# Performance work log

Measured on AMD Instinct MI355X. Metric: run time of the kernel, lower is better.

Reference implementation:

```python
import jax, jax.numpy as jnp
import numpy as np

D_MODEL = 512
H = 8
D_K = D_MODEL // H


def setup_inputs() -> dict:
    key = jax.random.key(0)
    ks = jax.random.split(key, 11)
    B, S = 2, 2048
    scale = 1.0 / np.sqrt(D_MODEL)
    return {
        "q": jax.random.normal(ks[0], (B, S, D_MODEL), jnp.float32),
        "v": jax.random.normal(ks[1], (B, S, D_MODEL), jnp.float32),
        "k": jax.random.normal(ks[2], (B, S, D_MODEL), jnp.float32),
        "w_q": jax.random.normal(ks[3], (D_MODEL, D_MODEL), jnp.float32) * scale,
        "b_q": jnp.zeros((D_MODEL,), jnp.float32),
        "w_k": jax.random.normal(ks[4], (D_MODEL, D_MODEL), jnp.float32) * scale,
        "b_k": jnp.zeros((D_MODEL,), jnp.float32),
        "w_v": jax.random.normal(ks[5], (D_MODEL, D_MODEL), jnp.float32) * scale,
        "b_v": jnp.zeros((D_MODEL,), jnp.float32),
        "w_o": jax.random.normal(ks[6], (D_MODEL, D_MODEL), jnp.float32) * scale,
        "b_o": jnp.zeros((D_MODEL,), jnp.float32),
    }


def reference(q, v, k, w_q, b_q, w_k, b_k, w_v, b_v, w_o, b_o):
    B, S, _ = q.shape
    # projections (nn.Linear: x @ W.T + b)
    query = q @ w_q.T + b_q
    key_t = k @ w_k.T + b_k
    value = v @ w_v.T + b_v
    # split heads: [B, S, H, D_K] -> [B, H, S, D_K]
    query = query.reshape(B, S, H, D_K).transpose(0, 2, 1, 3)
    key_t = key_t.reshape(B, S, H, D_K).transpose(0, 2, 1, 3)
    value = value.reshape(B, S, H, D_K).transpose(0, 2, 1, 3)
    # unfused attention: full [B, H, S, S] score matrix
    scores = jnp.einsum("bhqd,bhkd->bhqk", query, key_t) / jnp.sqrt(
        jnp.asarray(D_K, query.dtype)
    )
    attn = jax.nn.softmax(scores, axis=-1)  # dropout inactive in eval
    x = jnp.einsum("bhqk,bhkd->bhqd", attn, value)
    # merge heads and output projection
    x = x.transpose(0, 2, 1, 3).reshape(B, S, D_MODEL)
    return x @ w_o.T + b_o
```

## Files before the change

### kernel.cpp

```cpp
#include <hip/hip_runtime.h>
#include <hip/hip_bf16.h>


typedef __attribute__((ext_vector_type(8))) short short8;
typedef __attribute__((ext_vector_type(4))) short short4v;
typedef __attribute__((ext_vector_type(4))) float f32x4;
typedef __attribute__((ext_vector_type(2))) unsigned int uint2v;

#define DM 512
#define SEQ 2048
#define NROW 4096
#define LOG2E 1.44269504088896341f
#define MFMA(a, b, c) __builtin_amdgcn_mfma_f32_16x16x32_bf16(a, b, c, 0, 0, 0)
#define FENCE() __asm__ __volatile__("" ::: "memory")
#define WAITVM(n) __builtin_amdgcn_s_waitcnt(0x3F70 | (n))
#define WAITLGKM0() __builtin_amdgcn_s_waitcnt(0xC07F)
#define BARRIER() do { FENCE(); __builtin_amdgcn_s_barrier(); FENCE(); } while (0)

#if __has_builtin(__builtin_amdgcn_exp2f)
#define EXP2(x) __builtin_amdgcn_exp2f(x)
#else
#define EXP2(x) exp2f(x)
#endif

__device__ __forceinline__ float bf_bits2f(short s) {
    unsigned int u = ((unsigned int)(unsigned short)s) << 16;
    return __builtin_bit_cast(float, u);
}
__device__ __forceinline__ short f2bf_r(float f) {
    unsigned int u = __builtin_bit_cast(unsigned int, f) + 0x8000u;
    return (short)(u >> 16);
}
__device__ __forceinline__ unsigned int pack_bf16(float lo, float hi) {
    unsigned int ul = __builtin_bit_cast(unsigned int, lo) + 0x8000u;
    unsigned int uh = __builtin_bit_cast(unsigned int, hi) + 0x8000u;
    return __builtin_amdgcn_perm(uh, ul, 0x07060302u);
}

__device__ __forceinline__ void gload_lds16(const void* src, void* lds_dst) {
    __builtin_amdgcn_global_load_lds(
        (const __attribute__((address_space(1))) unsigned int*)src,
        (__attribute__((address_space(3))) unsigned int*)lds_dst, 16, 0, 0);
}

template <int ROWS, int NW, int SH>
__device__ __forceinline__ void stage_tile(const short* __restrict__ gsrc, size_t gstride,
                                           short* lds, int wave, int lane) {
    constexpr int ISSUES = ROWS * 8 / (64 * NW);
    #pragma unroll
    for (int i = 0; i < ISSUES; i++) {
        const int blk = i * NW + wave;
        const int g = blk * 64 + lane;
        const int row = g >> 3;
        const int cb = (g & 7) ^ ((row >> SH) & 7);
        gload_lds16(gsrc + (size_t)row * gstride + cb * 8, lds + (size_t)blk * 512);
    }
}

__device__ __forceinline__ bool detect_f32(const unsigned int* __restrict__ q, int* cnt_lds) {
    if (threadIdx.x == 0) *cnt_lds = 0;
    __syncthreads();
    int local = 0;
    for (int i = threadIdx.x; i < 1024; i += blockDim.x) {
        unsigned int lo = q[i] & 0x7FFFu;
        if (lo >= 0x3000u && lo < 0x4400u) local++;
    }
    if (local) atomicAdd(cnt_lds, local);
    __syncthreads();
    return *cnt_lds < 512;
}

struct ConvArgs { const void* src[11]; short* dst[11]; int n[11]; };
__global__ void convert_all(ConvArgs a) {
    __shared__ int cnt;
    const bool f32m = detect_f32((const unsigned int*)a.src[0], &cnt);
    if (!f32m) return;
    const int tid = blockIdx.x * 256 + threadIdx.x;
    const int stride = gridDim.x * 256;
    for (int s = 0; s < 11; s++) {
        const float4* sp = (const float4*)a.src[s];
        short4v* dp = (short4v*)a.dst[s];
        const int n4 = a.n[s] >> 2;
        for (int i = tid; i < n4; i += stride) {
            float4 v = sp[i];
            short4v o;
            o[0] = f2bf_r(v.x); o[1] = f2bf_r(v.y);
            o[2] = f2bf_r(v.z); o[3] = f2bf_r(v.w);
            dp[i] = o;
        }
    }
}

template <int MT>
__device__ __forceinline__ void gemm_core(const short* __restrict__ A,
                                          const short* __restrict__ W,
                                          int m0, int n0, short* Alds, short* Blds,
                                          int wave, int lane, f32x4 (&acc)[MT / 64][4]) {
    const int rc = lane & 15, quad = lane >> 4;
    const short* Ag = A + (size_t)m0 * DM;
    const short* Bg = W + (size_t)n0 * DM;
    constexpr int ABUF = MT * 64, BBUF = 64 * 64;
    constexpr int IN = MT * 8 / 256 + 2;
    constexpr int NITER = DM / 64;

    stage_tile<MT, 4, 0>(Ag, DM, Alds, wave, lane);
    stage_tile<64, 4, 0>(Bg, DM, Blds, wave, lane);
    stage_tile<MT, 4, 0>(Ag + 64, DM, Alds + ABUF, wave, lane);
    stage_tile<64, 4, 0>(Bg + 64, DM, Blds + BBUF, wave, lane);

    #pragma unroll
    for (int i = 0; i < NITER; i++) {
        const int cur = i % 3;
        if (i + 1 < NITER) WAITVM(IN); else WAITVM(0);
        BARRIER();
        if (i + 2 < NITER) {
            const int nb = (i + 2) % 3;
            stage_tile<MT, 4, 0>(Ag + (i + 2) * 64, DM, Alds + nb * ABUF, wave, lane);
            stage_tile<64, 4, 0>(Bg + (i + 2) * 64, DM, Blds + nb * BBUF, wave, lane);
        }
        const short* Ac = Alds + cur * ABUF;
        const short* Bc = Blds + cur * BBUF;
        #pragma unroll
        for (int h = 0; h < 2; h++) {
            short8 bf[4];
            #pragma unroll
            for (int nt = 0; nt < 4; nt++) {
                const int br = nt * 16 + rc;
                bf[nt] = *(const short8*)&Bc[br * 64 + (((quad + 4 * h) ^ (br & 7)) * 8)];
            }
            #pragma unroll
            for (int ms = 0; ms < MT / 64; ms++) {
                const int ar = wave * (MT / 4) + ms * 16 + rc;
                short8 af = *(const short8*)&Ac[ar * 64 + (((quad + 4 * h) ^ (ar & 7)) * 8)];
                #pragma unroll
                for (int nt = 0; nt < 4; nt++)
                    acc[ms][nt] = MFMA(af, bf[nt], acc[ms][nt]);
            }
        }
    }
}

struct QKVArgs {
    const short* Araw[3]; const short* Wraw[3]; const short* Braw[3];
    const short* Acv[3];  const short* Wcv[3];  const short* Bcv[3];
    short* Cq; short* Ck; short* Cv;
    const unsigned int* qraw;
};
__global__ __launch_bounds__(256, 2) void qkv_gemm(QKVArgs args) {
    __shared__ __align__(16) short Alds[3][128 * 64];
    __shared__ __align__(16) short Blds[3][64 * 64];
    __shared__ int cnt;
    const bool f32m = detect_f32(args.qraw, &cnt);
    const int z = blockIdx.z;
    const short* A    = f32m ? args.Acv[z] : args.Araw[z];
    const short* W    = f32m ? args.Wcv[z] : args.Wraw[z];
    const short* bias = f32m ? args.Bcv[z] : args.Braw[z];
    const int wave = threadIdx.x >> 6, lane = threadIdx.x & 63;
    const int rc = lane & 15, quad = lane >> 4;
    const int m0 = blockIdx.x * 128, n0 = blockIdx.y * 64;

    f32x4 acc[2][4] = {};
    gemm_core<128>(A, W, m0, n0, &Alds[0][0], &Blds[0][0], wave, lane, acc);

    if (z == 2) {
        const int hh = n0 >> 6;
        #pragma unroll
        for (int ms = 0; ms < 2; ms++) {
            const int mw = m0 + wave * 32 + ms * 16;
            const int b = mw >> 11, sb = (mw & 2047) + quad * 4;
            #pragma unroll
            for (int nt = 0; nt < 4; nt++) {
                const int d = nt * 16 + rc;
                const float bv = bf_bits2f(bias[n0 + d]);
                short4v pk;
                #pragma unroll
                for (int r = 0; r < 4; r++) pk[r] = f2bf_r(acc[ms][nt][r] + bv);
                *(short4v*)(args.Cv + ((size_t)((b * 8 + hh) * 64 + d)) * SEQ + sb) = pk;
            }
        }
    } else {
        short* C = (z == 0) ? args.Cq : args.Ck;
        const float sc = (z == 0) ? (0.125f * LOG2E) : 1.0f;
        #pragma unroll
        for (int ms = 0; ms < 2; ms++) {
            const int mw = m0 + wave * 32 + ms * 16;
            #pragma unroll
            for (int nt = 0; nt < 4; nt++) {
                const int col = n0 + nt * 16 + rc;
                const float bv = bf_bits2f(bias[col]);
                #pragma unroll
                for (int r = 0; r < 4; r++)
                    C[(size_t)(mw + quad * 4 + r) * DM + col] = f2bf_r((acc[ms][nt][r] + bv) * sc);
            }
        }
    }
}

__global__ __launch_bounds__(256, 2) void out_gemm(
    const short* __restrict__ A, const short* __restrict__ Wraw,
    const short* __restrict__ Wcv, const short* __restrict__ Braw,
    const short* __restrict__ Bcv, void* __restrict__ Cout,
    const unsigned int* __restrict__ qraw) {
    __shared__ __align__(16) short Alds[3][64 * 64];
    __shared__ __align__(16) short Blds[3][64 * 64];
    __shared__ int cnt;
    const bool f32m = detect_f32(qraw, &cnt);
    const short* W    = f32m ? Wcv : Wraw;
    const short* bias = f32m ? Bcv : Braw;
    const int wave = threadIdx.x >> 6, lane = threadIdx.x & 63;
    const int rc = lane & 15, quad = lane >> 4;
    const int m0 = blockIdx.x * 64, n0 = blockIdx.y * 64;
    f32x4 acc[1][4] = {};
    gemm_core<64>(A, W, m0, n0, &Alds[0][0], &Blds[0][0], wave, lane, acc);
    const int mw = m0 + wave * 16;
    #pragma unroll
    for (int nt = 0; nt < 4; nt++) {
        const int col = n0 + nt * 16 + rc;
        const float bv = bf_bits2f(bias[col]);
        #pragma unroll
        for (int r = 0; r < 4; r++) {
            const size_t idx = (size_t)(mw + quad * 4 + r) * DM + col;
            const float val = acc[0][nt][r] + bv;
            if (f32m) ((float*)Cout)[idx] = val;
            else      ((short*)Cout)[idx] = f2bf_r(val);
        }
    }
}

__global__ __launch_bounds__(256, 2) void attn_kernel(
    const short* __restrict__ Q, const short* __restrict__ K,
    const short* __restrict__ Vt, float* __restrict__ Opart,
    float* __restrict__ Lpart)
{
    __shared__ __align__(16) short Klds[3][64 * 64];
    __shared__ __align__(16) short Vlds[3][64 * 64];
    __shared__ __align__(16) short Plds[4][32 * 72];

    const int wave = threadIdx.x >> 6, lane = threadIdx.x & 63;
    const int rc = lane & 15, quad = lane >> 4;
    const int bh = blockIdx.y, z = blockIdx.z;
    const size_t baseQ = (size_t)(bh >> 3) * SEQ * DM + (size_t)(bh & 7) * 64;
    const short* Qb = Q + baseQ;
    const short* Kb = K + baseQ + (size_t)(z * 1024) * DM;
    const short* Vb = Vt + (size_t)bh * 64 * SEQ + z * 1024;
    const int q0 = blockIdx.x * 128 + wave * 32;

    short8 qa[2][2];
    #pragma unroll
    for (int ms = 0; ms < 2; ms++)
        #pragma unroll
        for (int h = 0; h < 2; h++)
            qa[ms][h] = *(const short8*)(Qb + (size_t)(q0 + ms * 16 + rc) * DM + h * 32 + quad * 8);

    short8 ones;
    #pragma unroll
    for (int j = 0; j < 8; j++) ones[j] = (short)0x3F80;

    f32x4 o[2][4] = {};
    f32x4 lsum[2] = {};
    short* Pw = &Plds[wave][0];

    int koff[4][2], voff[4][2];
    #pragma unroll
    for (int kt = 0; kt < 4; kt++) {
        const int row = rc * 4 + kt;
        #pragma unroll
        for (int h = 0; h < 2; h++)
            koff[kt][h] = row * 64 + (((quad + 4 * h) ^ (rc & 7)) * 8);
    }
    #pragma unroll
    for (int dt = 0; dt < 4; dt++) {
        const int row = dt * 16 + rc;
        #pragma unroll
        for (int h = 0; h < 2; h++)
            voff[dt][h] = row * 64 + (((quad + 4 * h) ^ (row & 7)) * 8);
    }

    stage_tile<64, 4, 2>(Kb, DM, &Klds[0][0], wave, lane);
    stage_tile<64, 4, 0>(Vb, SEQ, &Vlds[0][0], wave, lane);
    stage_tile<64, 4, 2>(Kb + (size_t)64 * DM, DM, &Klds[1][0], wave, lane);
    stage_tile<64, 4, 0>(Vb + 64, SEQ, &Vlds[1][0], wave, lane);

    #pragma unroll
    for (int it = 0; it < 16; it++) {
        const int cur = it % 3;
        if (it + 1 < 16) WAITVM(4); else WAITVM(0);
        BARRIER();
        if (it + 2 < 16) {
            const int k0n = (it + 2) * 64;
            const int nb = (it + 2) % 3;
            stage_tile<64, 4, 2>(Kb + (size_t)k0n * DM, DM, &Klds[nb][0], wave, lane);
            stage_tile<64, 4, 0>(Vb + k0n, SEQ, &Vlds[nb][0], wave, lane);
        }
        const short* Kt = &Klds[cur][0];
        const short* Vl = &Vlds[cur][0];

        short8 kf[4][2];
        #pragma unroll
        for (int kt = 0; kt < 4; kt++)
            #pragma unroll
            for (int h = 0; h < 2; h++)
                kf[kt][h] = *(const short8*)&Kt[koff[kt][h]];
        f32x4 s[2][4];
        #pragma unroll
        for (int ms = 0; ms < 2; ms++)
            #pragma unroll
            for (int kt = 0; kt < 4; kt++) {
                f32x4 t = {};
                t = MFMA(qa[ms][0], kf[kt][0], t);
                t = MFMA(qa[ms][1], kf[kt][1], t);
                s[ms][kt] = t;
            }
        #pragma unroll
        for (int ms = 0; ms < 2; ms++)
            #pragma unroll
            for (int r = 0; r < 4; r++) {
                uint2v pk;
                pk[0] = pack_bf16(EXP2(s[ms][0][r]), EXP2(s[ms][1][r]));
                pk[1] = pack_bf16(EXP2(s[ms][2][r]), EXP2(s[ms][3][r]));
                *(uint2v*)(&Pw[(ms * 16 + quad * 4 + r) * 72 + rc * 4]) = pk;
            }
        WAITLGKM0();
        short8 pa[2][2];
        #pragma unroll
        for (int ms = 0; ms < 2; ms++)
            #pragma unroll
            for (int h = 0; h < 2; h++)
                pa[ms][h] = *(const short8*)(&Pw[(ms * 16 + rc) * 72 + h * 32 + quad * 8]);
        #pragma unroll
        for (int ms = 0; ms < 2; ms++) {
            lsum[ms] = MFMA(pa[ms][0], ones, lsum[ms]);
            lsum[ms] = MFMA(pa[ms][1], ones, lsum[ms]);
        }
        #pragma unroll
        for (int dt = 0; dt < 4; dt++) {
            short8 v0 = *(const short8*)&Vl[voff[dt][0]];
            short8 v1 = *(const short8*)&Vl[voff[dt][1]];
            #pragma unroll
            for (int ms = 0; ms < 2; ms++) {
                o[ms][dt] = MFMA(pa[ms][0], v0, o[ms][dt]);
                o[ms][dt] = MFMA(pa[ms][1], v1, o[ms][dt]);
            }
        }
    }

    const size_t obase = ((size_t)(z * 16 + bh)) * SEQ;
    #pragma unroll
    for (int ms = 0; ms < 2; ms++) {
        const int qrow = q0 + ms * 16 + quad * 4;
        if (rc == 0) {
            #pragma unroll
            for (int r = 0; r < 4; r++)
                Lpart[obase + qrow + r] = lsum[ms][r];
        }
        #pragma unroll
        for (int dt = 0; dt < 4; dt++)
            #pragma unroll
            for (int r = 0; r < 4; r++)
                Opart[(obase + qrow + r) * 64 + dt * 16 + rc] = o[ms][dt][r];
    }
}

__global__ void attn_reduce(const float* __restrict__ Opart, const float* __restrict__ Lpart,
                            short* __restrict__ X) {
    const int idx = blockIdx.x * 256 + threadIdx.x;
    const int dq = idx & 15;
    const int bhq = idx >> 4;
    const int bh = bhq >> 11, q = bhq & 2047;
    const float4 o0 = ((const float4*)Opart)[(size_t)bhq * 16 + dq];
    const float4 o1 = ((const float4*)Opart)[(size_t)(bhq + 16 * SEQ) * 16 + dq];
    const float inv = 1.0f / (Lpart[bhq] + Lpart[bhq + 16 * SEQ]);
    short4v pk;
    pk[0] = f2bf_r((o0.x + o1.x) * inv);
    pk[1] = f2bf_r((o0.y + o1.y) * inv);
    pk[2] = f2bf_r((o0.z + o1.z) * inv);
    pk[3] = f2bf_r((o0.w + o1.w) * inv);
    const size_t row = (size_t)(bh >> 3) * SEQ + q;
    *(short4v*)(&X[row * DM + (bh & 7) * 64 + dq * 4]) = pk;
}

extern "C" void kernel_launch(void* const* d_in, const int* in_sizes, int n_in,
                              void* d_out, int out_size, void* d_ws, size_t ws_size,
                              hipStream_t stream) {
    char* ws = (char*)d_ws;
    const size_t SEQB = (size_t)NROW * DM * sizeof(short);
    const size_t WB   = (size_t)DM * DM * sizeof(short);
    const size_t BB   = (size_t)DM * sizeof(short);

    size_t off = 0;
    short* qc = (short*)(ws + off); off += SEQB;
    short* vc = (short*)(ws + off); off += SEQB;
    short* kc = (short*)(ws + off); off += SEQB;
    short* wq = (short*)(ws + off); off += WB;
    short* wk = (short*)(ws + off); off += WB;
    short* wv = (short*)(ws + off); off += WB;
    short* wo = (short*)(ws + off); off += WB;
    short* bq = (short*)(ws + off); off += BB;
    short* bk = (short*)(ws + off); off += BB;
    short* bv = (short*)(ws + off); off += BB;
    short* bo = (short*)(ws + off); off += BB;
    off = (off + 255) & ~(size_t)255;
    short* Qp  = (short*)(ws + off); off += SEQB;
    short* Kp  = (short*)(ws + off); off += SEQB;
    short* Vtp = (short*)(ws + off); off += SEQB;
    short* Xp  = (short*)(ws + off); off += SEQB;
    float* Opart = (float*)(ws + off); off += (size_t)2 * 16 * SEQ * 64 * sizeof(float);
    float* Lpart = (float*)(ws + off); off += (size_t)2 * 16 * SEQ * sizeof(float);

    ConvArgs ca;
    const void* srcs[11] = {d_in[0], d_in[1], d_in[2], d_in[3], d_in[5], d_in[7],
                            d_in[9], d_in[4], d_in[6], d_in[8], d_in[10]};
    short* dsts[11] = {qc, vc, kc, wq, wk, wv, wo, bq, bk, bv, bo};
    int ns[11] = {NROW * DM, NROW * DM, NROW * DM, DM * DM, DM * DM, DM * DM,
                  DM * DM, DM, DM, DM, DM};
    for (int i = 0; i < 11; i++) { ca.src[i] = srcs[i]; ca.dst[i] = dsts[i]; ca.n[i] = ns[i]; }
    convert_all<<<256, 256, 0, stream>>>(ca);

    QKVArgs qa;
    qa.Araw[0] = (const short*)d_in[0]; qa.Araw[1] = (const short*)d_in[2]; qa.Araw[2] = (const short*)d_in[1];
    qa.Wraw[0] = (const short*)d_in[3]; qa.Wraw[1] = (const short*)d_in[5]; qa.Wraw[2] = (const short*)d_in[7];
    qa.Braw[0] = (const short*)d_in[4]; qa.Braw[1] = (const short*)d_in[6]; qa.Braw[2] = (const short*)d_in[8];
    qa.Acv[0] = qc; qa.Acv[1] = kc; qa.Acv[2] = vc;
    qa.Wcv[0] = wq; qa.Wcv[1] = wk; qa.Wcv[2] = wv;
    qa.Bcv[0] = bq; qa.Bcv[1] = bk; qa.Bcv[2] = bv;
    qa.Cq = Qp; qa.Ck = Kp; qa.Cv = Vtp;
    qa.qraw = (const unsigned int*)d_in[0];
    qkv_gemm<<<dim3(NROW / 128, DM / 64, 3), 256, 0, stream>>>(qa);

    attn_kernel<<<dim3(SEQ / 128, 16, 2), 256, 0, stream>>>(Qp, Kp, Vtp, Opart, Lpart);
    attn_reduce<<<dim3(16 * SEQ * 16 / 256), 256, 0, stream>>>(Opart, Lpart, Xp);

    out_gemm<<<dim3(NROW / 64, DM / 64), 256, 0, stream>>>(
        Xp, (const short*)d_in[9], wo, (const short*)d_in[10], bo,
        d_out, (const unsigned int*)d_in[0]);
}
```

Before: 156.1 us.

## Fuse all stages into one persistent kernel with software grid barriers

Replaces the five launches (convert, QKV GEMM, attention, reduce, output GEMM) with a single persistent kernel of 256 blocks by 512 threads, separated by atomic grid barriers. The two key-halves of attention are now computed by two wave groups in the same block and combined through LDS, which removes the float partial buffers and the separate reduce pass. The aim is to cut launch overhead and global round-trips for the partials. In exchange it depends on all 256 blocks being co-resident, runs at lower occupancy with a 2-stage pipeline instead of 3, and each block runs the QKV GEMMs serially.

```diff
diff --git a/kernel.cpp b/kernel.cpp
--- a/kernel.cpp
+++ b/kernel.cpp
@@ -10,6 +10,7 @@
 #define DM 512
 #define SEQ 2048
 #define NROW 4096
+#define NBLK 256
 #define LOG2E 1.44269504088896341f
 #define MFMA(a, b, c) __builtin_amdgcn_mfma_f32_16x16x32_bf16(a, b, c, 0, 0, 0)
 #define FENCE() __asm__ __volatile__("" ::: "memory")
@@ -45,11 +46,11 @@
 
 template <int ROWS, int NW, int SH>
 __device__ __forceinline__ void stage_tile(const short* __restrict__ gsrc, size_t gstride,
-                                           short* lds, int wave, int lane) {
+                                           short* lds, int w, int lane) {
     constexpr int ISSUES = ROWS * 8 / (64 * NW);
     #pragma unroll
     for (int i = 0; i < ISSUES; i++) {
-        const int blk = i * NW + wave;
+        const int blk = i * NW + w;
         const int g = blk * 64 + lane;
         const int row = g >> 3;
         const int cb = (g & 7) ^ ((row >> SH) & 7);
@@ -57,326 +58,309 @@
     }
 }
 
-__device__ __forceinline__ bool detect_f32(const unsigned int* __restrict__ q, int* cnt_lds) {
-    if (threadIdx.x == 0) *cnt_lds = 0;
+__device__ __forceinline__ void grid_barrier(unsigned int* slot) {
     __syncthreads();
-    int local = 0;
-    for (int i = threadIdx.x; i < 1024; i += blockDim.x) {
-        unsigned int lo = q[i] & 0x7FFFu;
-        if (lo >= 0x3000u && lo < 0x4400u) local++;
-    }
-    if (local) atomicAdd(cnt_lds, local);
+    if (threadIdx.x == 0) {
+        __threadfence();
+        __hip_atomic_fetch_add(slot, 1u, __ATOMIC_RELEASE, __HIP_MEMORY_SCOPE_AGENT);
+        while (__hip_atomic_load(slot, __ATOMIC_ACQUIRE, __HIP_MEMORY_SCOPE_AGENT) < NBLK) {}
+        __threadfence();
+    }
     __syncthreads();
-    return *cnt_lds < 512;
-}
-
-struct ConvArgs { const void* src[11]; short* dst[11]; int n[11]; };
-__global__ void convert_all(ConvArgs a) {
-    __shared__ int cnt;
-    const bool f32m = detect_f32((const unsigned int*)a.src[0], &cnt);
-    if (!f32m) return;
-    const int tid = blockIdx.x * 256 + threadIdx.x;
-    const int stride = gridDim.x * 256;
-    for (int s = 0; s < 11; s++) {
-        const float4* sp = (const float4*)a.src[s];
-        short4v* dp = (short4v*)a.dst[s];
-        const int n4 = a.n[s] >> 2;
-        for (int i = tid; i < n4; i += stride) {
-            float4 v = sp[i];
-            short4v o;
-            o[0] = f2bf_r(v.x); o[1] = f2bf_r(v.y);
-            o[2] = f2bf_r(v.z); o[3] = f2bf_r(v.w);
-            dp[i] = o;
-        }
-    }
-}
-
-template <int MT>
-__device__ __forceinline__ void gemm_core(const short* __restrict__ A,
-                                          const short* __restrict__ W,
-                                          int m0, int n0, short* Alds, short* Blds,
-                                          int wave, int lane, f32x4 (&acc)[MT / 64][4]) {
+}
+
+struct FArgs {
+    const void* src[11]; short* dst[11]; int n[11];
+    const short* Araw[3]; const short* Wraw[3]; const short* Braw[3];
+    const short* Acv[3];  const short* Wcv[3];  const short* Bcv[3];
+    const short* WoRaw; const short* BoRaw; const short* WoCv; const short* BoCv;
+    short* Qp; short* Kp; short* Vtp; short* Xp;
+    void* out;
+    unsigned int* barr;
+};
+
+__device__ __forceinline__ void gemm8(const short* __restrict__ A,
+                                      const short* __restrict__ W,
+                                      int m0, int n0, short* SMEM,
+                                      int wave, int lane, f32x4 (&acc)[4]) {
     const int rc = lane & 15, quad = lane >> 4;
     const short* Ag = A + (size_t)m0 * DM;
     const short* Bg = W + (size_t)n0 * DM;
-    constexpr int ABUF = MT * 64, BBUF = 64 * 64;
-    constexpr int IN = MT * 8 / 256 + 2;
-    constexpr int NITER = DM / 64;
-
-    stage_tile<MT, 4, 0>(Ag, DM, Alds, wave, lane);
-    stage_tile<64, 4, 0>(Bg, DM, Blds, wave, lane);
-    stage_tile<MT, 4, 0>(Ag + 64, DM, Alds + ABUF, wave, lane);
-    stage_tile<64, 4, 0>(Bg + 64, DM, Blds + BBUF, wave, lane);
-
+    short* Alds = SMEM;
+    short* Blds = SMEM + 16384;
+    stage_tile<128, 8, 0>(Ag, DM, Alds, wave, lane);
+    stage_tile<64, 8, 0>(Bg, DM, Blds, wave, lane);
     #pragma unroll
-    for (int i = 0; i < NITER; i++) {
-        const int cur = i % 3;
-        if (i + 1 < NITER) WAITVM(IN); else WAITVM(0);
+    for (int i = 0; i < 8; i++) {
+        const int cur = i & 1;
+        if (i + 1 < 8) {
+            stage_tile<128, 8, 0>(Ag + (i + 1) * 64, DM, Alds + (cur ^ 1) * 8192, wave, lane);
+            stage_tile<64, 8, 0>(Bg + (i + 1) * 64, DM, Blds + (cur ^ 1) * 4096, wave, lane);
+            WAITVM(3);
+        } else {
+            WAITVM(0);
+        }
         BARRIER();
-        if (i + 2 < NITER) {
-            const int nb = (i + 2) % 3;
-            stage_tile<MT, 4, 0>(Ag + (i + 2) * 64, DM, Alds + nb * ABUF, wave, lane);
-            stage_tile<64, 4, 0>(Bg + (i + 2) * 64, DM, Blds + nb * BBUF, wave, lane);
-        }
-        const short* Ac = Alds + cur * ABUF;
-        const short* Bc = Blds + cur * BBUF;
+        const short* Ac = Alds + cur * 8192;
+        const short* Bc = Blds + cur * 4096;
+        const int ar = wave * 16 + rc;
         #pragma unroll
         for (int h = 0; h < 2; h++) {
-            short8 bf[4];
+            short8 af = *(const short8*)&Ac[ar * 64 + (((quad + 4 * h) ^ (ar & 7)) * 8)];
             #pragma unroll
             for (int nt = 0; nt < 4; nt++) {
                 const int br = nt * 16 + rc;
-                bf[nt] = *(const short8*)&Bc[br * 64 + (((quad + 4 * h) ^ (br & 7)) * 8)];
-            }
-            #pragma unroll
-            for (int ms = 0; ms < MT / 64; ms++) {
-                const int ar = wave * (MT / 4) + ms * 16 + rc;
-                short8 af = *(const short8*)&Ac[ar * 64 + (((quad + 4 * h) ^ (ar & 7)) * 8)];
-                #pragma unroll
-                for (int nt = 0; nt < 4; nt++)
-                    acc[ms][nt] = MFMA(af, bf[nt], acc[ms][nt]);
-            }
-        }
-    }
-}
-
-struct QKVArgs {
-    const short* Araw[3]; const short* Wraw[3]; const short* Braw[3];
-    const short* Acv[3];  const short* Wcv[3];  const short* Bcv[3];
-    short* Cq; short* Ck; short* Cv;
-    const unsigned int* qraw;
-};
-__global__ __launch_bounds__(256, 2) void qkv_gemm(QKVArgs args) {
-    __shared__ __align__(16) short Alds[3][128 * 64];
-    __shared__ __align__(16) short Blds[3][64 * 64];
+                short8 bf = *(const short8*)&Bc[br * 64 + (((quad + 4 * h) ^ (br & 7)) * 8)];
+                acc[nt] = MFMA(af, bf, acc[nt]);
+            }
+        }
+        BARRIER();
+    }
+}
+
+__global__ __launch_bounds__(512, 1) void fused_mha(FArgs a) {
+    extern __shared__ __align__(16) short SMEM[];
     __shared__ int cnt;
-    const bool f32m = detect_f32(args.qraw, &cnt);
-    const int z = blockIdx.z;
-    const short* A    = f32m ? args.Acv[z] : args.Araw[z];
-    const short* W    = f32m ? args.Wcv[z] : args.Wraw[z];
-    const short* bias = f32m ? args.Bcv[z] : args.Braw[z];
-    const int wave = threadIdx.x >> 6, lane = threadIdx.x & 63;
+    const int tid = threadIdx.x;
+    const int wave = tid >> 6, lane = tid & 63;
     const int rc = lane & 15, quad = lane >> 4;
-    const int m0 = blockIdx.x * 128, n0 = blockIdx.y * 64;
-
-    f32x4 acc[2][4] = {};
-    gemm_core<128>(A, W, m0, n0, &Alds[0][0], &Blds[0][0], wave, lane, acc);
-
-    if (z == 2) {
-        const int hh = n0 >> 6;
-        #pragma unroll
-        for (int ms = 0; ms < 2; ms++) {
-            const int mw = m0 + wave * 32 + ms * 16;
-            const int b = mw >> 11, sb = (mw & 2047) + quad * 4;
-            #pragma unroll
-            for (int nt = 0; nt < 4; nt++) {
-                const int d = nt * 16 + rc;
-                const float bv = bf_bits2f(bias[n0 + d]);
-                short4v pk;
-                #pragma unroll
-                for (int r = 0; r < 4; r++) pk[r] = f2bf_r(acc[ms][nt][r] + bv);
-                *(short4v*)(args.Cv + ((size_t)((b * 8 + hh) * 64 + d)) * SEQ + sb) = pk;
-            }
-        }
-    } else {
-        short* C = (z == 0) ? args.Cq : args.Ck;
-        const float sc = (z == 0) ? (0.125f * LOG2E) : 1.0f;
-        #pragma unroll
-        for (int ms = 0; ms < 2; ms++) {
-            const int mw = m0 + wave * 32 + ms * 16;
-            #pragma unroll
-            for (int nt = 0; nt < 4; nt++) {
-                const int col = n0 + nt * 16 + rc;
-                const float bv = bf_bits2f(bias[col]);
-                #pragma unroll
-                for (int r = 0; r < 4; r++)
-                    C[(size_t)(mw + quad * 4 + r) * DM + col] = f2bf_r((acc[ms][nt][r] + bv) * sc);
-            }
-        }
-    }
-}
-
-__global__ __launch_bounds__(256, 2) void out_gemm(
-    const short* __restrict__ A, const short* __restrict__ Wraw,
-    const short* __restrict__ Wcv, const short* __restrict__ Braw,
-    const short* __restrict__ Bcv, void* __restrict__ Cout,
-    const unsigned int* __restrict__ qraw) {
-    __shared__ __align__(16) short Alds[3][64 * 64];
-    __shared__ __align__(16) short Blds[3][64 * 64];
-    __shared__ int cnt;
-    const bool f32m = detect_f32(qraw, &cnt);
-    const short* W    = f32m ? Wcv : Wraw;
-    const short* bias = f32m ? Bcv : Braw;
-    const int wave = threadIdx.x >> 6, lane = threadIdx.x & 63;
-    const int rc = lane & 15, quad = lane >> 4;
-    const int m0 = blockIdx.x * 64, n0 = blockIdx.y * 64;
-    f32x4 acc[1][4] = {};
-    gemm_core<64>(A, W, m0, n0, &Alds[0][0], &Blds[0][0], wave, lane, acc);
-    const int mw = m0 + wave * 16;
-    #pragma unroll
-    for (int nt = 0; nt < 4; nt++) {
-        const int col = n0 + nt * 16 + rc;
-        const float bv = bf_bits2f(bias[col]);
-        #pragma unroll
-        for (int r = 0; r < 4; r++) {
-            const size_t idx = (size_t)(mw + quad * 4 + r) * DM + col;
-            const float val = acc[0][nt][r] + bv;
-            if (f32m) ((float*)Cout)[idx] = val;
-            else      ((short*)Cout)[idx] = f2bf_r(val);
-        }
-    }
-}
-
-__global__ __launch_bounds__(256, 2) void attn_kernel(
-    const short* __restrict__ Q, const short* __restrict__ K,
-    const short* __restrict__ Vt, float* __restrict__ Opart,
-    float* __restrict__ Lpart)
-{
-    __shared__ __align__(16) short Klds[3][64 * 64];
-    __shared__ __align__(16) short Vlds[3][64 * 64];
-    __shared__ __align__(16) short Plds[4][32 * 72];
-
-    const int wave = threadIdx.x >> 6, lane = threadIdx.x & 63;
-    const int rc = lane & 15, quad = lane >> 4;
-    const int bh = blockIdx.y, z = blockIdx.z;
-    const size_t baseQ = (size_t)(bh >> 3) * SEQ * DM + (size_t)(bh & 7) * 64;
-    const short* Qb = Q + baseQ;
-    const short* Kb = K + baseQ + (size_t)(z * 1024) * DM;
-    const short* Vb = Vt + (size_t)bh * 64 * SEQ + z * 1024;
-    const int q0 = blockIdx.x * 128 + wave * 32;
-
-    short8 qa[2][2];
-    #pragma unroll
-    for (int ms = 0; ms < 2; ms++)
-        #pragma unroll
-        for (int h = 0; h < 2; h++)
-            qa[ms][h] = *(const short8*)(Qb + (size_t)(q0 + ms * 16 + rc) * DM + h * 32 + quad * 8);
-
-    short8 ones;
-    #pragma unroll
-    for (int j = 0; j < 8; j++) ones[j] = (short)0x3F80;
-
-    f32x4 o[2][4] = {};
-    f32x4 lsum[2] = {};
-    short* Pw = &Plds[wave][0];
-
-    int koff[4][2], voff[4][2];
-    #pragma unroll
-    for (int kt = 0; kt < 4; kt++) {
-        const int row = rc * 4 + kt;
-        #pragma unroll
-        for (int h = 0; h < 2; h++)
-            koff[kt][h] = row * 64 + (((quad + 4 * h) ^ (rc & 7)) * 8);
-    }
-    #pragma unroll
-    for (int dt = 0; dt < 4; dt++) {
-        const int row = dt * 16 + rc;
-        #pragma unroll
-        for (int h = 0; h < 2; h++)
-            voff[dt][h] = row * 64 + (((quad + 4 * h) ^ (row & 7)) * 8);
-    }
-
-    stage_tile<64, 4, 2>(Kb, DM, &Klds[0][0], wave, lane);
-    stage_tile<64, 4, 0>(Vb, SEQ, &Vlds[0][0], wave, lane);
-    stage_tile<64, 4, 2>(Kb + (size_t)64 * DM, DM, &Klds[1][0], wave, lane);
-    stage_tile<64, 4, 0>(Vb + 64, SEQ, &Vlds[1][0], wave, lane);
-
-    #pragma unroll
-    for (int it = 0; it < 16; it++) {
-        const int cur = it % 3;
-        if (it + 1 < 16) WAITVM(4); else WAITVM(0);
-        BARRIER();
-        if (it + 2 < 16) {
-            const int k0n = (it + 2) * 64;
-            const int nb = (it + 2) % 3;
-            stage_tile<64, 4, 2>(Kb + (size_t)k0n * DM, DM, &Klds[nb][0], wave, lane);
-            stage_tile<64, 4, 0>(Vb + k0n, SEQ, &Vlds[nb][0], wave, lane);
-        }
-        const short* Kt = &Klds[cur][0];
-        const short* Vl = &Vlds[cur][0];
-
-        short8 kf[4][2];
-        #pragma unroll
-        for (int kt = 0; kt < 4; kt++)
+    const int blk = blockIdx.x;
+
+    if (tid == 0) cnt = 0;
+    __syncthreads();
+    {
+        const unsigned int* q = (const unsigned int*)a.src[0];
+        int local = 0;
+        for (int i = tid; i < 1024; i += 512) {
+            unsigned int lo = q[i] & 0x7FFFu;
+            if (lo >= 0x3000u && lo < 0x4400u) local++;
+        }
+        if (local) atomicAdd(&cnt, local);
+    }
+    __syncthreads();
+    const bool f32m = (cnt < 512);
+
+    if (f32m) {
+        const int gtid = blk * 512 + tid;
+        for (int s = 0; s < 11; s++) {
+            const float4* sp = (const float4*)a.src[s];
+            short4v* dp = (short4v*)a.dst[s];
+            const int n4 = a.n[s] >> 2;
+            for (int i = gtid; i < n4; i += NBLK * 512) {
+                float4 v = sp[i];
+                short4v o;
+                o[0] = f2bf_r(v.x); o[1] = f2bf_r(v.y);
+                o[2] = f2bf_r(v.z); o[3] = f2bf_r(v.w);
+                dp[i] = o;
+            }
+        }
+    }
+    grid_barrier(&a.barr[0]);
+
+    {
+        const int m0 = (blk >> 3) * 128, n0 = (blk & 7) * 64;
+        for (int z = 0; z < 3; z++) {
+            const short* A    = f32m ? a.Acv[z] : a.Araw[z];
+            const short* W    = f32m ? a.Wcv[z] : a.Wraw[z];
+            const short* bias = f32m ? a.Bcv[z] : a.Braw[z];
+            f32x4 acc[4] = {};
+            gemm8(A, W, m0, n0, SMEM, wave, lane, acc);
+            const int mw = m0 + wave * 16;
+            if (z == 2) {
+                const int hh = n0 >> 6;
+                const int b = mw >> 11, sb = (mw & 2047) + quad * 4;
+                #pragma unroll
+                for (int nt = 0; nt < 4; nt++) {
+                    const int d = nt * 16 + rc;
+                    const float bv = bf_bits2f(bias[n0 + d]);
+                    short4v pk;
+                    #pragma unroll
+                    for (int r = 0; r < 4; r++) pk[r] = f2bf_r(acc[nt][r] + bv);
+                    *(short4v*)(a.Vtp + ((size_t)((b * 8 + hh) * 64 + d)) * SEQ + sb) = pk;
+                }
+            } else {
+                short* C = (z == 0) ? a.Qp : a.Kp;
+                const float sc = (z == 0) ? (0.125f * LOG2E) : 1.0f;
+                #pragma unroll
+                for (int nt = 0; nt < 4; nt++) {
+                    const int col = n0 + nt * 16 + rc;
+                    const float bv = bf_bits2f(bias[col]);
+                    #pragma unroll
+                    for (int r = 0; r < 4; r++)
+                        C[(size_t)(mw + quad * 4 + r) * DM + col] = f2bf_r((acc[nt][r] + bv) * sc);
+                }
+            }
+            __syncthreads();
+        }
+    }
+    grid_barrier(&a.barr[1]);
+
+    {
+        const int bh = blk & 15, qb = blk >> 4;
+        const int g = wave >> 2, wg = wave & 3;
+        const size_t baseQ = (size_t)(bh >> 3) * SEQ * DM + (size_t)(bh & 7) * 64;
+        const short* Qb = a.Qp + baseQ;
+        const short* Kb = a.Kp + baseQ + (size_t)(g * 1024) * DM;
+        const short* Vb = a.Vtp + (size_t)bh * 64 * SEQ + g * 1024;
+        const int q0 = qb * 128 + wg * 32;
+
+        short* Kg = SMEM + g * 8192;
+        short* Vg = SMEM + 16384 + g * 8192;
+        short* Pw = SMEM + 32768 + wave * 2304;
+
+        short8 qa[2][2];
+        #pragma unroll
+        for (int ms = 0; ms < 2; ms++)
             #pragma unroll
             for (int h = 0; h < 2; h++)
-                kf[kt][h] = *(const short8*)&Kt[koff[kt][h]];
-        f32x4 s[2][4];
-        #pragma unroll
-        for (int ms = 0; ms < 2; ms++)
-            #pragma unroll
-            for (int kt = 0; kt < 4; kt++) {
-                f32x4 t = {};
-                t = MFMA(qa[ms][0], kf[kt][0], t);
-                t = MFMA(qa[ms][1], kf[kt][1], t);
-                s[ms][kt] = t;
-            }
-        #pragma unroll
-        for (int ms = 0; ms < 2; ms++)
+                qa[ms][h] = *(const short8*)(Qb + (size_t)(q0 + ms * 16 + rc) * DM + h * 32 + quad * 8);
+
+        short8 ones;
+        #pragma unroll
+        for (int j = 0; j < 8; j++) ones[j] = (short)0x3F80;
+
+        f32x4 o[2][4] = {};
+        f32x4 lsum[2] = {};
+
+        int koff[4][2], voff[4][2];
+        #pragma unroll
+        for (int kt = 0; kt < 4; kt++) {
+            const int row = rc * 4 + kt;
+            #pragma unroll
+            for (int h = 0; h < 2; h++)
+                koff[kt][h] = row * 64 + (((quad + 4 * h) ^ (rc & 7)) * 8);
+        }
+        #pragma unroll
+        for (int dt = 0; dt < 4; dt++) {
+            const int row = dt * 16 + rc;
+            #pragma unroll
+            for (int h = 0; h < 2; h++)
+                voff[dt][h] = row * 64 + (((quad + 4 * h) ^ (row & 7)) * 8);
+        }
+
+        stage_tile<64, 4, 2>(Kb, DM, Kg, wg, lane);
+        stage_tile<64, 4, 0>(Vb, SEQ, Vg, wg, lane);
+
+        #pragma unroll 2
+        for (int it = 0; it < 16; it++) {
+            const int cur = it & 1;
+            if (it + 1 < 16) {
+                const int k0n = (it + 1) * 64;
+                stage_tile<64, 4, 2>(Kb + (size_t)k0n * DM, DM, Kg + (cur ^ 1) * 4096, wg, lane);
+                stage_tile<64, 4, 0>(Vb + k0n, SEQ, Vg + (cur ^ 1) * 4096, wg, lane);
+                WAITVM(4);
+            } else {
+                WAITVM(0);
+            }
+            BARRIER();
+            const short* Kt = Kg + cur * 4096;
+            const short* Vl = Vg + cur * 4096;
+
+            short8 kf[4][2];
+            #pragma unroll
+            for (int kt = 0; kt < 4; kt++)
+                #pragma unroll
+                for (int h = 0; h < 2; h++)
+                    kf[kt][h] = *(const short8*)&Kt[koff[kt][h]];
+            f32x4 s[2][4];
+            #pragma unroll
+            for (int ms = 0; ms < 2; ms++)
+                #pragma unroll
+                for (int kt = 0; kt < 4; kt++) {
+                    f32x4 t = {};
+                    t = MFMA(qa[ms][0], kf[kt][0], t);
+                    t = MFMA(qa[ms][1], kf[kt][1], t);
+                    s[ms][kt] = t;
+                }
+            #pragma unroll
+            for (int ms = 0; ms < 2; ms++)
+                #pragma unroll
+                for (int r = 0; r < 4; r++) {
+                    uint2v pk;
+                    pk[0] = pack_bf16(EXP2(s[ms][0][r]), EXP2(s[ms][1][r]));
+                    pk[1] = pack_bf16(EXP2(s[ms][2][r]), EXP2(s[ms][3][r]));
+                    *(uint2v*)(&Pw[(ms * 16 + quad * 4 + r) * 72 + rc * 4]) = pk;
+                }
+            WAITLGKM0();
+            short8 pa[2][2];
+            #pragma unroll
+            for (int ms = 0; ms < 2; ms++)
+                #pragma unroll
+                for (int h = 0; h < 2; h++)
+                    pa[ms][h] = *(const short8*)(&Pw[(ms * 16 + rc) * 72 + h * 32 + quad * 8]);
+            #pragma unroll
+            for (int ms = 0; ms < 2; ms++) {
+                lsum[ms] = MFMA(pa[ms][0], ones, lsum[ms]);
+                lsum[ms] = MFMA(pa[ms][1], ones, lsum[ms]);
+            }
+            #pragma unroll
+            for (int dt = 0; dt < 4; dt++) {
+                short8 v0 = *(const short8*)&Vl[voff[dt][0]];
+                short8 v1 = *(const short8*)&Vl[voff[dt][1]];
+                #pragma unroll
+                for (int ms = 0; ms < 2; ms++) {
+                    o[ms][dt] = MFMA(pa[ms][0], v0, o[ms][dt]);
+                    o[ms][dt] = MFMA(pa[ms][1], v1, o[ms][dt]);
+                }
+            }
+            BARRIER();
+        }
+
+        float* OLf = (float*)SMEM;
+        float* Lb  = OLf + 128 * 64;
+        __syncthreads();
+        if (g == 1) {
+            #pragma unroll
+            for (int ms = 0; ms < 2; ms++)
+                #pragma unroll
+                for (int r = 0; r < 4; r++) {
+                    const int ql = wg * 32 + ms * 16 + quad * 4 + r;
+                    if (rc == 0) Lb[ql] = lsum[ms][r];
+                    #pragma unroll
+                    for (int dt = 0; dt < 4; dt++)
+                        OLf[ql * 64 + dt * 16 + rc] = o[ms][dt][r];
+                }
+        }
+        __syncthreads();
+        if (g == 0) {
+            #pragma unroll
+            for (int ms = 0; ms < 2; ms++)
+                #pragma unroll
+                for (int r = 0; r < 4; r++) {
+                    const int ql = wg * 32 + ms * 16 + quad * 4 + r;
+                    const float inv = 1.0f / (lsum[ms][r] + Lb[ql]);
+                    const size_t row = (size_t)(bh >> 3) * SEQ + qb * 128 + ql;
+                    #pragma unroll
+                    for (int dt = 0; dt < 4; dt++) {
+                        const float tot = o[ms][dt][r] + OLf[ql * 64 + dt * 16 + rc];
+                        a.Xp[row * DM + (bh & 7) * 64 + dt * 16 + rc] = f2bf_r(tot * inv);
+                    }
+                }
+        }
+        __syncthreads();
+    }
+    grid_barrier(&a.barr[2]);
+
+    {
+        const short* W    = f32m ? a.WoCv : a.WoRaw;
+        const short* bias = f32m ? a.BoCv : a.BoRaw;
+        const int m0 = (blk >> 3) * 128, n0 = (blk & 7) * 64;
+        f32x4 acc[4] = {};
+        gemm8(a.Xp, W, m0, n0, SMEM, wave, lane, acc);
+        const int mw = m0 + wave * 16;
+        #pragma unroll
+        for (int nt = 0; nt < 4; nt++) {
+            const int col = n0 + nt * 16 + rc;
+            const float bv = bf_bits2f(bias[col]);
             #pragma unroll
             for (int r = 0; r < 4; r++) {
-                uint2v pk;
-                pk[0] = pack_bf16(EXP2(s[ms][0][r]), EXP2(s[ms][1][r]));
-                pk[1] = pack_bf16(EXP2(s[ms][2][r]), EXP2(s[ms][3][r]));
-                *(uint2v*)(&Pw[(ms * 16 + quad * 4 + r) * 72 + rc * 4]) = pk;
-            }
-        WAITLGKM0();
-        short8 pa[2][2];
-        #pragma unroll
-        for (int ms = 0; ms < 2; ms++)
-            #pragma unroll
-            for (int h = 0; h < 2; h++)
-                pa[ms][h] = *(const short8*)(&Pw[(ms * 16 + rc) * 72 + h * 32 + quad * 8]);
-        #pragma unroll
-        for (int ms = 0; ms < 2; ms++) {
-            lsum[ms] = MFMA(pa[ms][0], ones, lsum[ms]);
-            lsum[ms] = MFMA(pa[ms][1], ones, lsum[ms]);
-        }
-        #pragma unroll
-        for (int dt = 0; dt < 4; dt++) {
-            short8 v0 = *(const short8*)&Vl[voff[dt][0]];
-            short8 v1 = *(const short8*)&Vl[voff[dt][1]];
-            #pragma unroll
-            for (int ms = 0; ms < 2; ms++) {
-                o[ms][dt] = MFMA(pa[ms][0], v0, o[ms][dt]);
-                o[ms][dt] = MFMA(pa[ms][1], v1, o[ms][dt]);
-            }
-        }
-    }
-
-    const size_t obase = ((size_t)(z * 16 + bh)) * SEQ;
-    #pragma unroll
-    for (int ms = 0; ms < 2; ms++) {
-        const int qrow = q0 + ms * 16 + quad * 4;
-        if (rc == 0) {
-            #pragma unroll
-            for (int r = 0; r < 4; r++)
-                Lpart[obase + qrow + r] = lsum[ms][r];
-        }
-        #pragma unroll
-        for (int dt = 0; dt < 4; dt++)
-            #pragma unroll
-            for (int r = 0; r < 4; r++)
-                Opart[(obase + qrow + r) * 64 + dt * 16 + rc] = o[ms][dt][r];
-    }
-}
-
-__global__ void attn_reduce(const float* __restrict__ Opart, const float* __restrict__ Lpart,
-                            short* __restrict__ X) {
-    const int idx = blockIdx.x * 256 + threadIdx.x;
-    const int dq = idx & 15;
-    const int bhq = idx >> 4;
-    const int bh = bhq >> 11, q = bhq & 2047;
-    const float4 o0 = ((const float4*)Opart)[(size_t)bhq * 16 + dq];
-    const float4 o1 = ((const float4*)Opart)[(size_t)(bhq + 16 * SEQ) * 16 + dq];
-    const float inv = 1.0f / (Lpart[bhq] + Lpart[bhq + 16 * SEQ]);
-    short4v pk;
-    pk[0] = f2bf_r((o0.x + o1.x) * inv);
-    pk[1] = f2bf_r((o0.y + o1.y) * inv);
-    pk[2] = f2bf_r((o0.z + o1.z) * inv);
-    pk[3] = f2bf_r((o0.w + o1.w) * inv);
-    const size_t row = (size_t)(bh >> 3) * SEQ + q;
-    *(short4v*)(&X[row * DM + (bh & 7) * 64 + dq * 4]) = pk;
+                const size_t idx = (size_t)(mw + quad * 4 + r) * DM + col;
+                const float val = acc[nt][r] + bv;
+                if (f32m) ((float*)a.out)[idx] = val;
+                else      ((short*)a.out)[idx] = f2bf_r(val);
+            }
+        }
+    }
 }
 
 extern "C" void kernel_launch(void* const* d_in, const int* in_sizes, int n_in,
@@ -387,7 +371,8 @@
     const size_t WB   = (size_t)DM * DM * sizeof(short);
     const size_t BB   = (size_t)DM * sizeof(short);
 
-    size_t off = 0;
+    unsigned int* barr = (unsigned int*)ws;
+    size_t off = 256;
     short* qc = (short*)(ws + off); off += SEQB;
     short* vc = (short*)(ws + off); off += SEQB;
     short* kc = (short*)(ws + off); off += SEQB;
@@ -404,33 +389,27 @@
     short* Kp  = (short*)(ws + off); off += SEQB;
     short* Vtp = (short*)(ws + off); off += SEQB;
     short* Xp  = (short*)(ws + off); off += SEQB;
-    float* Opart = (float*)(ws + off); off += (size_t)2 * 16 * SEQ * 64 * sizeof(float);
-    float* Lpart = (float*)(ws + off); off += (size_t)2 * 16 * SEQ * sizeof(float);
-
-    ConvArgs ca;
+
+    hipMemsetAsync(barr, 0, 3 * sizeof(unsigned int), stream);
+
+    FArgs fa;
     const void* srcs[11] = {d_in[0], d_in[1], d_in[2], d_in[3], d_in[5], d_in[7],
                             d_in[9], d_in[4], d_in[6], d_in[8], d_in[10]};
     short* dsts[11] = {qc, vc, kc, wq, wk, wv, wo, bq, bk, bv, bo};
     int ns[11] = {NROW * DM, NROW * DM, NROW * DM, DM * DM, DM * DM, DM * DM,
                   DM * DM, DM, DM, DM, DM};
-    for (int i = 0; i < 11; i++) { ca.src[i] = srcs[i]; ca.dst[i] = dsts[i]; ca.n[i] = ns[i]; }
-    convert_all<<<256, 256, 0, stream>>>(ca);
-
-    QKVArgs qa;
-    qa.Araw[0] = (const short*)d_in[0]; qa.Araw[1] = (const short*)d_in[2]; qa.Araw[2] = (const short*)d_in[1];
-    qa.Wraw[0] = (const short*)d_in[3]; qa.Wraw[1] = (const short*)d_in[5]; qa.Wraw[2] = (const short*)d_in[7];
-    qa.Braw[0] = (const short*)d_in[4]; qa.Braw[1] = (const short*)d_in[6]; qa.Braw[2] = (const short*)d_in[8];
-    qa.Acv[0] = qc; qa.Acv[1] = kc; qa.Acv[2] = vc;
-    qa.Wcv[0] = wq; qa.Wcv[1] = wk; qa.Wcv[2] = wv;
-    qa.Bcv[0] = bq; qa.Bcv[1] = bk; qa.Bcv[2] = bv;
-    qa.Cq = Qp; qa.Ck = Kp; qa.Cv = Vtp;
-    qa.qraw = (const unsigned int*)d_in[0];
-    qkv_gemm<<<dim3(NROW / 128, DM / 64, 3), 256, 0, stream>>>(qa);
-
-    attn_kernel<<<dim3(SEQ / 128, 16, 2), 256, 0, stream>>>(Qp, Kp, Vtp, Opart, Lpart);
-    attn_reduce<<<dim3(16 * SEQ * 16 / 256), 256, 0, stream>>>(Opart, Lpart, Xp);
-
-    out_gemm<<<dim3(NROW / 64, DM / 64), 256, 0, stream>>>(
-        Xp, (const short*)d_in[9], wo, (const short*)d_in[10], bo,
-        d_out, (const unsigned int*)d_in[0]);
-}
+    for (int i = 0; i < 11; i++) { fa.src[i] = srcs[i]; fa.dst[i] = dsts[i]; fa.n[i] = ns[i]; }
+    fa.Araw[0] = (const short*)d_in[0]; fa.Araw[1] = (const short*)d_in[2]; fa.Araw[2] = (const short*)d_in[1];
+    fa.Wraw[0] = (const short*)d_in[3]; fa.Wraw[1] = (const short*)d_in[5]; fa.Wraw[2] = (const short*)d_in[7];
+    fa.Braw[0] = (const short*)d_in[4]; fa.Braw[1] = (const short*)d_in[6]; fa.Braw[2] = (const short*)d_in[8];
+    fa.Acv[0] = qc; fa.Acv[1] = kc; fa.Acv[2] = vc;
+    fa.Wcv[0] = wq; fa.Wcv[1] = wk; fa.Wcv[2] = wv;
+    fa.Bcv[0] = bq; fa.Bcv[1] = bk; fa.Bcv[2] = bv;
+    fa.WoRaw = (const short*)d_in[9]; fa.BoRaw = (const short*)d_in[10];
+    fa.WoCv = wo; fa.BoCv = bo;
+    fa.Qp = Qp; fa.Kp = Kp; fa.Vtp = Vtp; fa.Xp = Xp;
+    fa.out = d_out;
+    fa.barr = barr;
+
+    fused_mha<<<NBLK, 512, 51200 * sizeof(short), stream>>>(fa);
+}
```

Result: slower. 241.0 us (+54.4%).
